# Kernel tuning notes

Hardware: AMD Instinct MI355X
Metric: run time of the kernel (lower is better)

Reference implementation:

```python
import jax, jax.numpy as jnp
import numpy as np

CH = 16
R = 9  # reduced_res = ceil(log2(256)+1)


def grid_sample_bilinear(P, gx, gy):
    """torch.F.grid_sample, mode=bilinear, align_corners=True, zeros padding.
    P: (C, H, W); gx indexes width (last axis), gy indexes height. Returns (C, N)."""
    C, H, W = P.shape
    ix = (gx + 1.0) * 0.5 * (W - 1)
    iy = (gy + 1.0) * 0.5 * (H - 1)
    x0 = jnp.floor(ix)
    y0 = jnp.floor(iy)
    wx = ix - x0
    wy = iy - y0
    x0i = jnp.clip(x0.astype(jnp.int32), 0, W - 1)
    x1i = jnp.clip(x0i + 1, 0, W - 1)
    y0i = jnp.clip(y0.astype(jnp.int32), 0, H - 1)
    y1i = jnp.clip(y0i + 1, 0, H - 1)
    v00 = P[:, y0i, x0i]
    v01 = P[:, y0i, x1i]
    v10 = P[:, y1i, x0i]
    v11 = P[:, y1i, x1i]
    return (v00 * (1 - wx) * (1 - wy) + v01 * wx * (1 - wy)
            + v10 * (1 - wx) * wy + v11 * wx * wy)


def plane_feature(P, gx, gy, c_int):
    # sample -> (N, ch, R), then cosine-basis numerical integration over R
    s = grid_sample_bilinear(P, gx, gy)              # (R*ch, N)
    s = s.T.reshape(-1, CH, R)                       # (N, ch, R)
    c = (c_int + 1.0) * 0.5 * (2.0 ** (R - 1) - 1.0)  # (N,)
    freqs = (2.0 ** jnp.arange(R, dtype=jnp.float32)) - 0.5
    basis = jnp.cos(jnp.pi * (c[:, None] + 0.5) * freqs / (2.0 ** R))  # (N, R)
    return 2.0 * jnp.einsum('nr,ncr->nc', basis, s)  # (N, ch)


def setup_inputs() -> dict:
    key = jax.random.key(0)
    k1, k2, k3, k4 = jax.random.split(key, 4)
    coords = jax.random.uniform(k1, (524288, 3), dtype=jnp.float32) * 2.0 - 1.0
    Pu = jax.random.normal(k2, (R * CH, 256, 256), dtype=jnp.float32) * 0.1
    Pv = jax.random.normal(k3, (R * CH, 256, 256), dtype=jnp.float32) * 0.1
    Pw = jax.random.normal(k4, (R * CH, 256, 256), dtype=jnp.float32) * 0.1
    return {"coords": coords, "Pu": Pu, "Pv": Pv, "Pw": Pw}


def reference(coords, Pu, Pv, Pw):
    # Pu sampled with (coord1, coord2), integrated along coord0; etc.
    fu = plane_feature(Pu, coords[:, 1], coords[:, 2], coords[:, 0])
    fv = plane_feature(Pv, coords[:, 0], coords[:, 2], coords[:, 1])
    fw = plane_feature(Pw, coords[:, 0], coords[:, 1], coords[:, 2])
    return fu + fv + fw  # (N, ch)
```

## Files before the change

### kernel.cpp

```cpp
#include <hip/hip_runtime.h>
#include <hip/hip_bf16.h>

#define CHN 16
#define RF 9
#define HWDIM 256
#define POSN (HWDIM * HWDIM)
#define NBINS 32768

typedef _Float16 half2_t __attribute__((ext_vector_type(2)));

__device__ __forceinline__ half2_t u2h(uint32_t u) {
    union { uint32_t u; half2_t h; } x; x.u = u; return x.h;
}
__device__ __forceinline__ uint32_t f2h(float f) {
    union { _Float16 h; uint16_t u; } x; x.h = (_Float16)f; return (uint32_t)x.u;
}
__device__ __forceinline__ float h2f(uint32_t u) {
    union { uint16_t u; _Float16 h; } x; x.u = (uint16_t)u; return (float)x.h;
}

#if __has_builtin(__builtin_amdgcn_fdot2)
__device__ __forceinline__ float DOT2(half2_t a, half2_t b, float c) {
    return __builtin_amdgcn_fdot2(a, b, c, false);
}
#else
__device__ __forceinline__ float DOT2(half2_t a, half2_t b, float c) {
    return fmaf((float)a.x, (float)b.x, fmaf((float)a.y, (float)b.y, c));
}
#endif

__device__ __forceinline__ uint32_t part1by2(uint32_t x) {
    x &= 0x3ffu;
    x = (x | (x << 16)) & 0x030000FFu;
    x = (x | (x << 8))  & 0x0300F00Fu;
    x = (x | (x << 4))  & 0x030C30C3u;
    x = (x | (x << 2))  & 0x09249249u;
    return x;
}
__device__ __forceinline__ uint32_t morton_key(float c0, float c1, float c2) {
    int q0 = min(31, max(0, (int)((c0 + 1.f) * 16.f)));
    int q1 = min(31, max(0, (int)((c1 + 1.f) * 16.f)));
    int q2 = min(31, max(0, (int)((c2 + 1.f) * 16.f)));
    return (part1by2((uint32_t)q0) << 2) | (part1by2((uint32_t)q1) << 1) | part1by2((uint32_t)q2);
}

__device__ __forceinline__ void pack_tile16(int tile,
                                            const float* __restrict__ Pu,
                                            const float* __restrict__ Pv,
                                            const float* __restrict__ Pw,
                                            uint4* __restrict__ A,
                                            uint32_t* __restrict__ B, int t) {
    int p = tile >> 12;
    int pos = ((tile & 4095) << 4) + (t >> 4);
    int cc = t & 15;
    const float* P = (p == 0) ? Pu : ((p == 1) ? Pv : Pw);
    const float* Pc = P + (size_t)(cc * RF) * POSN + pos;
    uint32_t w[4];
#pragma unroll
    for (int j = 0; j < 4; ++j) {
        float v0 = Pc[(size_t)(2 * j) * POSN];
        float v1 = Pc[(size_t)(2 * j + 1) * POSN];
        w[j] = f2h(v0) | (f2h(v1) << 16);
    }
    A[((size_t)p * POSN + pos) * CHN + cc] = make_uint4(w[0], w[1], w[2], w[3]);
    uint32_t h8 = f2h(Pc[(size_t)8 * POSN]);
    uint32_t other = __shfl_xor(h8, 1);
    if (!(cc & 1)) {
        B[((size_t)p * POSN + pos) * 8 + (cc >> 1)] = h8 | (other << 16);
    }
}

__global__ __launch_bounds__(256) void fuse_hist(const float* __restrict__ Pu,
                                                 const float* __restrict__ Pv,
                                                 const float* __restrict__ Pw,
                                                 uint4* __restrict__ A,
                                                 uint32_t* __restrict__ B,
                                                 const float* __restrict__ coords,
                                                 uint32_t* __restrict__ hist,
                                                 int N, int npack, int tile_lo) {
    int b = blockIdx.x, t = threadIdx.x;
    if (b < npack) {
        pack_tile16(tile_lo + b, Pu, Pv, Pw, A, B, t);
    } else {
        int n = (b - npack) * 256 + t;
        if (n < N) {
            float c0 = coords[3 * n], c1 = coords[3 * n + 1], c2 = coords[3 * n + 2];
            atomicAdd(&hist[morton_key(c0, c1, c2)], 1u);
        }
    }
}

__global__ __launch_bounds__(256) void fuse_scan(const float* __restrict__ Pu,
                                                 const float* __restrict__ Pv,
                                                 const float* __restrict__ Pw,
                                                 uint4* __restrict__ A,
                                                 uint32_t* __restrict__ B,
                                                 uint32_t* __restrict__ hist,
                                                 int npack, int tile_lo) {
    int b = blockIdx.x, t = threadIdx.x;
    if (b == 0) {
        __shared__ uint32_t sh[256];
        const int PER = NBINS / 256;
        int base = t * PER;
        uint32_t s = 0;
        for (int i = 0; i < PER; ++i) s += hist[base + i];
        sh[t] = s;
        __syncthreads();
        for (int off = 1; off < 256; off <<= 1) {
            uint32_t v = (t >= off) ? sh[t - off] : 0u;
            __syncthreads();
            sh[t] += v;
            __syncthreads();
        }
        uint32_t run = sh[t] - s;
        for (int i = 0; i < PER; ++i) {
            uint32_t h = hist[base + i];
            hist[base + i] = run;
            run += h;
        }
    } else {
        pack_tile16(tile_lo + (b - 1), Pu, Pv, Pw, A, B, t);
    }
}

__global__ __launch_bounds__(256) void fuse_scatter(const float* __restrict__ Pu,
                                                    const float* __restrict__ Pv,
                                                    const float* __restrict__ Pw,
                                                    uint4* __restrict__ A,
                                                    uint32_t* __restrict__ B,
                                                    const float* __restrict__ coords,
                                                    uint32_t* __restrict__ hist,
                                                    float4* __restrict__ sorted,
                                                    int N, int npack, int tile_lo) {
    int b = blockIdx.x, t = threadIdx.x;
    if (b < npack) {
        pack_tile16(tile_lo + b, Pu, Pv, Pw, A, B, t);
    } else {
        int n = (b - npack) * 256 + t;
        if (n < N) {
            float c0 = coords[3 * n], c1 = coords[3 * n + 1], c2 = coords[3 * n + 2];
            uint32_t key = morton_key(c0, c1, c2);
            uint32_t dst = atomicAdd(&hist[key], 1u);
            sorted[dst] = make_float4(c0, c1, c2, __uint_as_float((uint32_t)n));
        }
    }
}

__global__ __launch_bounds__(256) void triplane_f16v2(const float4* __restrict__ sorted,
                                                      const uint4* __restrict__ A,
                                                      const uint32_t* __restrict__ B,
                                                      float* __restrict__ out, int N, int nblk) {
    __shared__ float4 pts[32];
    __shared__ uint32_t meta[32 * 40];
    int blk = blockIdx.x;
    {
        int q = nblk >> 3, r = nblk & 7;
        int xcd = blk & 7, local = blk >> 3;
        blk = (xcd < r ? xcd * (q + 1) : r * (q + 1) + (xcd - r) * q) + local;
    }
    int base = blk * 32;
    int t = threadIdx.x;
    if (t < 32) {
        int i = base + t;
        pts[t] = (i < N) ? sorted[i] : make_float4(0.f, 0.f, 0.f, __uint_as_float(0u));
    }
    __syncthreads();
    if (t < 128 && (t & 3) < 3) {
        int pt = t >> 2, p = t & 3;
        float4 c = pts[pt];
        float gx = (p == 0) ? c.y : c.x;
        float gy = (p == 2) ? c.y : c.z;
        float ci = (p == 0) ? c.x : ((p == 1) ? c.y : c.z);
        float ix = (gx + 1.f) * 127.5f;
        float iy = (gy + 1.f) * 127.5f;
        float x0f = floorf(ix), y0f = floorf(iy);
        float wx = ix - x0f, wy = iy - y0f;
        int x0 = min(max((int)x0f, 0), HWDIM - 1);
        int y0 = min(max((int)y0f, 0), HWDIM - 1);
        int x1 = min(x0 + 1, HWDIM - 1);
        int y1 = min(y0 + 1, HWDIM - 1);
        uint32_t* m = &meta[pt * 40 + p * 13];
        float cv = (ci + 1.f) * 127.5f + 0.5f;
        float bb[9];
#pragma unroll
        for (int r = 0; r < 9; ++r) {
            const float k = 3.14159265358979f * ((float)(1 << r) - 0.5f) * (1.f / 512.f);
            bb[r] = __cosf(cv * k);
        }
#pragma unroll
        for (int j = 0; j < 4; ++j) m[j] = f2h(bb[2 * j]) | (f2h(bb[2 * j + 1]) << 16);
        m[4] = __float_as_uint(bb[8]);
        m[5] = __float_as_uint((1.f - wx) * (1.f - wy));
        m[6] = __float_as_uint(wx * (1.f - wy));
        m[7] = __float_as_uint((1.f - wx) * wy);
        m[8] = __float_as_uint(wx * wy);
        m[9]  = (uint32_t)(y0 * HWDIM + x0) * 256u;
        m[10] = (uint32_t)(y0 * HWDIM + x1) * 256u;
        m[11] = (uint32_t)(y1 * HWDIM + x0) * 256u;
        m[12] = (uint32_t)(y1 * HWDIM + x1) * 256u;
    }
    __syncthreads();
    int cc = t & 15, slot = t >> 4;
    const char* Ab = (const char*)A;
    const char* Bb = (const char*)B;
    const uint32_t bofs = ((uint32_t)(cc >> 1) << 2);
#pragma unroll
    for (int half = 0; half < 2; ++half) {
        int pt = slot + half * 16;
        int gi = base + pt;
        float acc = 0.f;
#pragma unroll
        for (int p = 0; p < 3; ++p) {
            const uint32_t* m = &meta[pt * 40 + p * 13];
            half2_t b01 = u2h(m[0]), b23 = u2h(m[1]), b45 = u2h(m[2]), b67 = u2h(m[3]);
            float b8 = __uint_as_float(m[4]);
            const char* Apl = Ab + (size_t)p * ((size_t)POSN * 256);
            const char* Bpl = Bb + (size_t)p * ((size_t)POSN * 32);
            float ps = 0.f;
#pragma unroll
            for (int k = 0; k < 4; ++k) {
                uint32_t ob = m[9 + k];
                uint4 a = *(const uint4*)(Apl + ob + cc * 16);
                uint32_t bw = *(const uint32_t*)(Bpl + (ob >> 3) + bofs);
                float v8 = h2f((cc & 1) ? (bw >> 16) : (bw & 0xffffu));
                float s = b8 * v8;
                s = DOT2(u2h(a.x), b01, s);
                s = DOT2(u2h(a.y), b23, s);
                s = DOT2(u2h(a.z), b45, s);
                s = DOT2(u2h(a.w), b67, s);
                ps = fmaf(__uint_as_float(m[5 + k]), s, ps);
            }
            acc += ps;
        }
        if (gi < N) {
            uint32_t n = __float_as_uint(pts[pt].w);
            out[(size_t)n * CHN + cc] = 2.f * acc;
        }
    }
}

__global__ __launch_bounds__(256) void triplane_direct(const float* __restrict__ coords,
                                                       const float* __restrict__ Pu,
                                                       const float* __restrict__ Pv,
                                                       const float* __restrict__ Pw,
                                                       float* __restrict__ out, int N) {
    int tid = blockIdx.x * blockDim.x + threadIdx.x;
    int n = tid >> 4;
    if (n >= N) return;
    int cc = tid & 15;
    float c0 = coords[3 * n + 0];
    float c1 = coords[3 * n + 1];
    float c2 = coords[3 * n + 2];
    float acc = 0.f;
#pragma unroll
    for (int p = 0; p < 3; ++p) {
        const float* P = (p == 0) ? Pu : ((p == 1) ? Pv : Pw);
        float gx = (p == 0) ? c1 : c0;
        float gy = (p == 2) ? c1 : c2;
        float ci = (p == 0) ? c0 : ((p == 1) ? c1 : c2);
        float ix = (gx + 1.f) * 127.5f;
        float iy = (gy + 1.f) * 127.5f;
        float x0f = floorf(ix), y0f = floorf(iy);
        float wx = ix - x0f, wy = iy - y0f;
        int x0 = min(max((int)x0f, 0), HWDIM - 1);
        int y0 = min(max((int)y0f, 0), HWDIM - 1);
        int x1 = min(x0 + 1, HWDIM - 1);
        int y1 = min(y0 + 1, HWDIM - 1);
        float cv = (ci + 1.f) * 127.5f + 0.5f;
        float w00 = (1.f - wx) * (1.f - wy), w01 = wx * (1.f - wy);
        float w10 = (1.f - wx) * wy, w11 = wx * wy;
        int p00 = y0 * HWDIM + x0, p01 = y0 * HWDIM + x1;
        int p10 = y1 * HWDIM + x0, p11 = y1 * HWDIM + x1;
#pragma unroll
        for (int r = 0; r < RF; ++r) {
            const float k = 3.14159265358979f * ((float)(1 << r) - 0.5f) / 512.f;
            float b = __cosf(cv * k);
            const float* Pc = P + (size_t)(cc * RF + r) * POSN;
            float v = w00 * Pc[p00] + w01 * Pc[p01] + w10 * Pc[p10] + w11 * Pc[p11];
            acc = fmaf(b, v, acc);
        }
    }
    out[(size_t)n * CHN + cc] = 2.f * acc;
}

extern "C" void kernel_launch(void* const* d_in, const int* in_sizes, int n_in,
                              void* d_out, int out_size, void* d_ws, size_t ws_size,
                              hipStream_t stream) {
    const float* coords = (const float*)d_in[0];
    const float* Pu = (const float*)d_in[1];
    const float* Pv = (const float*)d_in[2];
    const float* Pw = (const float*)d_in[3];
    float* out = (float*)d_out;
    int N = in_sizes[0] / 3;

    size_t offA = 0;
    size_t szA = (size_t)3 * POSN * CHN * sizeof(uint4);
    size_t offB = offA + szA;
    size_t szB = (size_t)3 * POSN * 8 * sizeof(uint32_t);
    size_t offS = offB + szB;
    size_t szS = (size_t)N * sizeof(float4);
    size_t offH = offS + szS;
    size_t szH = (size_t)NBINS * sizeof(uint32_t);
    size_t need = offH + szH;

    if (ws_size >= need) {
        char* ws = (char*)d_ws;
        uint4* A = (uint4*)(ws + offA);
        uint32_t* B = (uint32_t*)(ws + offB);
        float4* sorted = (float4*)(ws + offS);
        uint32_t* hist = (uint32_t*)(ws + offH);

        int tblk = (3 * POSN) / 16;
        int s1 = tblk / 3;
        int s2 = tblk / 3;
        int s3 = tblk - s1 - s2;
        int hblk = (N + 255) / 256;

        hipMemsetAsync(hist, 0, szH, stream);
        fuse_hist<<<s1 + hblk, 256, 0, stream>>>(Pu, Pv, Pw, A, B, coords, hist, N, s1, 0);
        fuse_scan<<<1 + s2, 256, 0, stream>>>(Pu, Pv, Pw, A, B, hist, s2, s1);
        fuse_scatter<<<s3 + hblk, 256, 0, stream>>>(Pu, Pv, Pw, A, B, coords, hist, sorted,
                                                    N, s3, s1 + s2);
        int nblk = (N + 31) / 32;
        triplane_f16v2<<<nblk, 256, 0, stream>>>(sorted, A, B, out, N, nblk);
    } else {
        int threads = N * CHN;
        triplane_direct<<<(threads + 255) / 256, 256, 0, stream>>>(coords, Pu, Pv, Pw, out, N);
    }
}
```

Baseline: 204.1 us.

## Stage plane repacking through LDS with 128-position tiles for coalesced I/O

The plane repacking now processes 128 positions per block. Each thread handles 8 channels, reading the source planes with 128 contiguous floats per warp instead of 16, and stages the packed half-precision words in padded shared memory. The block then writes A and B out linearly in coalesced stores. This targets poorly coalesced global reads and strided writes in the pack step. It costs extra LDS, a barrier and fewer, larger pack blocks, and the shared arrays are also allocated in histogram blocks, which may lower occupancy there.

```diff
diff --git a/kernel.cpp b/kernel.cpp
--- a/kernel.cpp
+++ b/kernel.cpp
@@ -44,29 +44,48 @@
     return (part1by2((uint32_t)q0) << 2) | (part1by2((uint32_t)q1) << 1) | part1by2((uint32_t)q2);
 }
 
-__device__ __forceinline__ void pack_tile16(int tile,
-                                            const float* __restrict__ Pu,
-                                            const float* __restrict__ Pv,
-                                            const float* __restrict__ Pw,
-                                            uint4* __restrict__ A,
-                                            uint32_t* __restrict__ B, int t) {
-    int p = tile >> 12;
-    int pos = ((tile & 4095) << 4) + (t >> 4);
-    int cc = t & 15;
+__device__ __forceinline__ void pack_tile(int tile,
+                                          const float* __restrict__ Pu,
+                                          const float* __restrict__ Pv,
+                                          const float* __restrict__ Pw,
+                                          uint4* __restrict__ A,
+                                          uint32_t* __restrict__ B,
+                                          int t, uint4* LA, uint32_t* LB) {
+    int p = tile >> 9;
+    int pos_base = (tile & 511) * 128;
+    int pos = t & 127;
+    int ch = (t >> 7) * 8;
     const float* P = (p == 0) ? Pu : ((p == 1) ? Pv : Pw);
-    const float* Pc = P + (size_t)(cc * RF) * POSN + pos;
-    uint32_t w[4];
-#pragma unroll
-    for (int j = 0; j < 4; ++j) {
-        float v0 = Pc[(size_t)(2 * j) * POSN];
-        float v1 = Pc[(size_t)(2 * j + 1) * POSN];
-        w[j] = f2h(v0) | (f2h(v1) << 16);
-    }
-    A[((size_t)p * POSN + pos) * CHN + cc] = make_uint4(w[0], w[1], w[2], w[3]);
-    uint32_t h8 = f2h(Pc[(size_t)8 * POSN]);
-    uint32_t other = __shfl_xor(h8, 1);
-    if (!(cc & 1)) {
-        B[((size_t)p * POSN + pos) * 8 + (cc >> 1)] = h8 | (other << 16);
+    const float* Pc0 = P + pos_base + pos;
+    uint32_t r8 = 0;
+#pragma unroll
+    for (int c = 0; c < 8; ++c) {
+        int cc = ch + c;
+        const float* Pc = Pc0 + (size_t)(cc * RF) * POSN;
+        uint32_t w[4];
+#pragma unroll
+        for (int j = 0; j < 4; ++j) {
+            float v0 = Pc[(size_t)(2 * j) * POSN];
+            float v1 = Pc[(size_t)(2 * j + 1) * POSN];
+            w[j] = f2h(v0) | (f2h(v1) << 16);
+        }
+        LA[pos * 17 + cc] = make_uint4(w[0], w[1], w[2], w[3]);
+        uint32_t h8 = f2h(Pc[(size_t)8 * POSN]);
+        if (c & 1) { r8 |= (h8 << 16); LB[pos * 9 + (cc >> 1)] = r8; }
+        else r8 = h8;
+    }
+    __syncthreads();
+    uint4* Aout = A + ((size_t)p * POSN + pos_base) * CHN;
+#pragma unroll
+    for (int it = 0; it < 8; ++it) {
+        int i = it * 256 + t;
+        Aout[i] = LA[(i >> 4) * 17 + (i & 15)];
+    }
+    uint32_t* Bout = B + ((size_t)p * POSN + pos_base) * 8;
+#pragma unroll
+    for (int it = 0; it < 4; ++it) {
+        int i = it * 256 + t;
+        Bout[i] = LB[(i >> 3) * 9 + (i & 7)];
     }
 }
 
@@ -78,9 +97,11 @@
                                                  const float* __restrict__ coords,
                                                  uint32_t* __restrict__ hist,
                                                  int N, int npack, int tile_lo) {
+    __shared__ uint4 LA[128 * 17];
+    __shared__ uint32_t LB[128 * 9];
     int b = blockIdx.x, t = threadIdx.x;
     if (b < npack) {
-        pack_tile16(tile_lo + b, Pu, Pv, Pw, A, B, t);
+        pack_tile(tile_lo + b, Pu, Pv, Pw, A, B, t, LA, LB);
     } else {
         int n = (b - npack) * 256 + t;
         if (n < N) {
@@ -97,6 +118,8 @@
                                                  uint32_t* __restrict__ B,
                                                  uint32_t* __restrict__ hist,
                                                  int npack, int tile_lo) {
+    __shared__ uint4 LA[128 * 17];
+    __shared__ uint32_t LB[128 * 9];
     int b = blockIdx.x, t = threadIdx.x;
     if (b == 0) {
         __shared__ uint32_t sh[256];
@@ -119,7 +142,7 @@
             run += h;
         }
     } else {
-        pack_tile16(tile_lo + (b - 1), Pu, Pv, Pw, A, B, t);
+        pack_tile(tile_lo + (b - 1), Pu, Pv, Pw, A, B, t, LA, LB);
     }
 }
 
@@ -132,9 +155,11 @@
                                                     uint32_t* __restrict__ hist,
                                                     float4* __restrict__ sorted,
                                                     int N, int npack, int tile_lo) {
+    __shared__ uint4 LA[128 * 17];
+    __shared__ uint32_t LB[128 * 9];
     int b = blockIdx.x, t = threadIdx.x;
     if (b < npack) {
-        pack_tile16(tile_lo + b, Pu, Pv, Pw, A, B, t);
+        pack_tile(tile_lo + b, Pu, Pv, Pw, A, B, t, LA, LB);
     } else {
         int n = (b - npack) * 256 + t;
         if (n < N) {
@@ -310,7 +335,7 @@
         float4* sorted = (float4*)(ws + offS);
         uint32_t* hist = (uint32_t*)(ws + offH);
 
-        int tblk = (3 * POSN) / 16;
+        int tblk = (3 * POSN) / 128;
         int s1 = tblk / 3;
         int s2 = tblk / 3;
         int s3 = tblk - s1 - s2;
```

After: 173.0 us. 15.2% less time.

## Pack plane tiles through shared-memory transpose with 128-position tiles

Applied to the files above, without the earlier changes.

Replaces the per-thread 16-position packing of fp32 planes into fp16 channel-interleaved arrays with a 128-position tile. Each block loads rows with coalesced float4 reads, converts them to fp16 in LDS, then transposes and writes the A and B arrays with coalesced stores. The aim is to remove the strided scalar global reads of the previous packer. In exchange, each packing block uses about 38 KB of LDS and a barrier, which may lower occupancy for the fused histogram and scatter blocks that share the kernel.

```diff
diff --git a/kernel.cpp b/kernel.cpp
--- a/kernel.cpp
+++ b/kernel.cpp
@@ -6,6 +6,7 @@
 #define HWDIM 256
 #define POSN (HWDIM * HWDIM)
 #define NBINS 32768
+#define TPOS 128
 
 typedef _Float16 half2_t __attribute__((ext_vector_type(2)));
 
@@ -44,31 +45,52 @@
     return (part1by2((uint32_t)q0) << 2) | (part1by2((uint32_t)q1) << 1) | part1by2((uint32_t)q2);
 }
 
-__device__ __forceinline__ void pack_tile16(int tile,
-                                            const float* __restrict__ Pu,
-                                            const float* __restrict__ Pv,
-                                            const float* __restrict__ Pw,
-                                            uint4* __restrict__ A,
-                                            uint32_t* __restrict__ B, int t) {
-    int p = tile >> 12;
-    int pos = ((tile & 4095) << 4) + (t >> 4);
-    int cc = t & 15;
+__device__ __forceinline__ void pack_tile128(int tile,
+                                             const float* __restrict__ Pu,
+                                             const float* __restrict__ Pv,
+                                             const float* __restrict__ Pw,
+                                             uint4* __restrict__ A,
+                                             uint32_t* __restrict__ B,
+                                             int t, uint32_t* LHw) {
+    int p = tile >> 9;
+    int pos_base = (tile & 511) * TPOS;
     const float* P = (p == 0) ? Pu : ((p == 1) ? Pv : Pw);
-    const float* Pc = P + (size_t)(cc * RF) * POSN + pos;
-    uint32_t w[4];
-#pragma unroll
-    for (int j = 0; j < 4; ++j) {
-        float v0 = Pc[(size_t)(2 * j) * POSN];
-        float v1 = Pc[(size_t)(2 * j + 1) * POSN];
-        w[j] = f2h(v0) | (f2h(v1) << 16);
-    }
-    A[((size_t)p * POSN + pos) * CHN + cc] = make_uint4(w[0], w[1], w[2], w[3]);
-    uint32_t h8 = f2h(Pc[(size_t)8 * POSN]);
-    uint32_t other = __shfl_xor(h8, 1);
-    if (!(cc & 1)) {
-        B[((size_t)p * POSN + pos) * 8 + (cc >> 1)] = h8 | (other << 16);
-    }
-}
+#pragma unroll
+    for (int it = 0; it < 18; ++it) {
+        int j = it * 256 + t;
+        int row = j >> 5;
+        int col = j & 31;
+        const float* rp = P + (size_t)row * POSN + pos_base;
+        float4 v = ((const float4*)rp)[col];
+        LHw[row * 66 + col * 2 + 0] = f2h(v.x) | (f2h(v.y) << 16);
+        LHw[row * 66 + col * 2 + 1] = f2h(v.z) | (f2h(v.w) << 16);
+    }
+    __syncthreads();
+    const unsigned short* LH = (const unsigned short*)LHw;
+    uint4* Aout = A + ((size_t)p * POSN + pos_base) * CHN;
+#pragma unroll
+    for (int it = 0; it < 8; ++it) {
+        int i = it * 256 + t;
+        int pos = i >> 4, cc = i & 15;
+        const unsigned short* base = LH + (size_t)cc * 9 * 132 + pos;
+        uint32_t w0 = (uint32_t)base[0 * 132] | ((uint32_t)base[1 * 132] << 16);
+        uint32_t w1 = (uint32_t)base[2 * 132] | ((uint32_t)base[3 * 132] << 16);
+        uint32_t w2 = (uint32_t)base[4 * 132] | ((uint32_t)base[5 * 132] << 16);
+        uint32_t w3 = (uint32_t)base[6 * 132] | ((uint32_t)base[7 * 132] << 16);
+        Aout[i] = make_uint4(w0, w1, w2, w3);
+    }
+    uint32_t* Bout = B + ((size_t)p * POSN + pos_base) * 8;
+#pragma unroll
+    for (int it = 0; it < 4; ++it) {
+        int i = it * 256 + t;
+        int pos = i >> 3, g = i & 7;
+        uint32_t lo = LH[((size_t)(2 * g) * 9 + 8) * 132 + pos];
+        uint32_t hi = LH[((size_t)(2 * g + 1) * 9 + 8) * 132 + pos];
+        Bout[i] = lo | (hi << 16);
+    }
+}
+
+#define LHW_WORDS (144 * 66)
 
 __global__ __launch_bounds__(256) void fuse_hist(const float* __restrict__ Pu,
                                                  const float* __restrict__ Pv,
@@ -78,9 +100,10 @@
                                                  const float* __restrict__ coords,
                                                  uint32_t* __restrict__ hist,
                                                  int N, int npack, int tile_lo) {
+    __shared__ uint32_t LHw[LHW_WORDS];
     int b = blockIdx.x, t = threadIdx.x;
     if (b < npack) {
-        pack_tile16(tile_lo + b, Pu, Pv, Pw, A, B, t);
+        pack_tile128(tile_lo + b, Pu, Pv, Pw, A, B, t, LHw);
     } else {
         int n = (b - npack) * 256 + t;
         if (n < N) {
@@ -97,6 +120,7 @@
                                                  uint32_t* __restrict__ B,
                                                  uint32_t* __restrict__ hist,
                                                  int npack, int tile_lo) {
+    __shared__ uint32_t LHw[LHW_WORDS];
     int b = blockIdx.x, t = threadIdx.x;
     if (b == 0) {
         __shared__ uint32_t sh[256];
@@ -119,7 +143,7 @@
             run += h;
         }
     } else {
-        pack_tile16(tile_lo + (b - 1), Pu, Pv, Pw, A, B, t);
+        pack_tile128(tile_lo + (b - 1), Pu, Pv, Pw, A, B, t, LHw);
     }
 }
 
@@ -132,9 +156,10 @@
                                                     uint32_t* __restrict__ hist,
                                                     float4* __restrict__ sorted,
                                                     int N, int npack, int tile_lo) {
+    __shared__ uint32_t LHw[LHW_WORDS];
     int b = blockIdx.x, t = threadIdx.x;
     if (b < npack) {
-        pack_tile16(tile_lo + b, Pu, Pv, Pw, A, B, t);
+        pack_tile128(tile_lo + b, Pu, Pv, Pw, A, B, t, LHw);
     } else {
         int n = (b - npack) * 256 + t;
         if (n < N) {
@@ -310,7 +335,7 @@
         float4* sorted = (float4*)(ws + offS);
         uint32_t* hist = (uint32_t*)(ws + offH);
 
-        int tblk = (3 * POSN) / 16;
+        int tblk = (3 * POSN) / TPOS;
         int s1 = tblk / 3;
         int s2 = tblk / 3;
         int s3 = tblk - s1 - s2;
```

Result: faster. 177.0 us (-13.2%).
